# Performance work log

Measured on AMD Instinct MI355X. Metric: run time of the kernel, lower is better.

The kernel has to match this reference:

```python
import jax, jax.numpy as jnp
import numpy as np

DIM = 768
NUM_HEADS = 12
HEAD_DIM = DIM // NUM_HEADS
SCALE = HEAD_DIM ** -0.5
KEEP_NUM = 160


def setup_inputs() -> dict:
    key = jax.random.key(0)
    k0, k1, k2, k3 = jax.random.split(key, 4)
    B, N, C = 64, 197, DIM
    x = jax.random.normal(k0, (B, N, C), dtype=jnp.float32)
    # torch nn.Linear weights: [out_features, in_features]
    qkv_w = jax.random.normal(k1, (3 * C, C), dtype=jnp.float32) * (C ** -0.5)
    proj_w = jax.random.normal(k2, (C, C), dtype=jnp.float32) * (C ** -0.5)
    proj_b = jax.random.normal(k3, (C,), dtype=jnp.float32) * 0.01
    return {"x": x, "qkv_w": qkv_w, "proj_w": proj_w, "proj_b": proj_b}


def reference(x, qkv_w, proj_w, proj_b):
    B, N, C = x.shape
    H, D = NUM_HEADS, HEAD_DIM
    # qkv: [B, N, 3, H, D] -> q,k,v each [B, H, N, D]
    qkv = (x @ qkv_w.T).reshape(B, N, 3, H, D)
    qkv = jnp.transpose(qkv, (2, 0, 3, 1, 4))
    q, k, v = qkv[0], qkv[1], qkv[2]
    # raw pre-softmax scores [B, H, N, N]
    attn = jnp.einsum('bhnd,bhmd->bhnm', q, k) * SCALE
    # SUM_ABS_1: CLS row of scores, abs-summed over heads -> [B, N]
    attn_weight = jnp.sum(jnp.abs(attn[:, :, 0, :]), axis=1)
    # top_pool: keep top KEEP_NUM tokens by weight, indices sorted ascending
    _, idx = jax.lax.top_k(attn_weight, KEEP_NUM)
    keep_index = jnp.sort(idx, axis=-1)
    # standard attention
    attn = jax.nn.softmax(attn, axis=-1)
    out = jnp.einsum('bhnm,bhmd->bhnd', attn, v)
    out = jnp.transpose(out, (0, 2, 1, 3)).reshape(B, N, C)
    out = out @ proj_w.T + proj_b
    return out, keep_index
```

## Files before the change

kernel.cpp:

```cpp
#include <hip/hip_runtime.h>
#include <hip/hip_bf16.h>


#define BB 64
#define NN 197
#define CC 768
#define HH 12
#define DD 64
#define KEEP 160
#define SCALE_F 0.125f
#define OUT0_ELEMS ((size_t)BB * NN * CC)
#define VST 212

typedef __attribute__((ext_vector_type(8))) short bf16x8_t;
typedef __attribute__((ext_vector_type(4))) float f32x4_t;

__device__ __forceinline__ float b2f(unsigned short u) {
  union { unsigned u; float f; } cv; cv.u = (unsigned)u << 16; return cv.f;
}
__device__ __forceinline__ unsigned short f2b(float f) {
  union { float f; unsigned u; } cv; cv.f = f;
  return (unsigned short)((cv.u + 0x7FFFu + ((cv.u >> 16) & 1u)) >> 16);
}
__device__ __forceinline__ float ldmix(const void* p, size_t i, int f32) {
  return f32 ? ((const float*)p)[i] : b2f(((const unsigned short*)p)[i]);
}
__device__ __forceinline__ bf16x8_t ld8(const unsigned short* p) {
  short4 a = *(const short4*)p;
  short4 b = *(const short4*)(p + 4);
  bf16x8_t v = {a.x, a.y, a.z, a.w, b.x, b.y, b.z, b.w};
  return v;
}

__global__ void detect_kernel(const void* x, int* flag) {
  __shared__ int cnt;
  if (threadIdx.x == 0) cnt = 0;
  __syncthreads();
  const unsigned short* u = (const unsigned short*)x;
  int wild = 0;
  for (int i = threadIdx.x; i < 4096; i += 256) {
    int e = (u[i] >> 7) & 0xFF;
    wild += (e >= 140);
  }
  atomicAdd(&cnt, wild);
  __syncthreads();
  if (threadIdx.x == 0) *flag = (cnt > 100) ? 1 : 0;
}

__global__ void cvt_all(const void* qkv_w, const void* proj_w, const void* proj_b,
                        unsigned short* wb, unsigned short* pw, float* pbf,
                        const int* flag) {
  const int W3 = 3 * CC * CC, W1 = CC * CC;
  int i = blockIdx.x * 256 + threadIdx.x;
  const int f32 = *flag;
  if (i < W3) {
    wb[i] = f32 ? f2b(((const float*)qkv_w)[i]) : ((const unsigned short*)qkv_w)[i];
  } else if (i < W3 + W1) {
    int j = i - W3;
    pw[j] = f32 ? f2b(((const float*)proj_w)[j]) : ((const unsigned short*)proj_w)[j];
  } else if (i < W3 + W1 + CC) {
    int j = i - W3 - W1;
    pbf[j] = ldmix(proj_b, j, f32);
  }
}

__global__ void cvt_x(const void* __restrict__ x, size_t elem_off,
                      unsigned short* __restrict__ xb, int n8,
                      const int* __restrict__ flag) {
  const int i = blockIdx.x * 256 + threadIdx.x;
  if (i >= n8) return;
  const size_t src = elem_off + (size_t)i * 8;
  bf16x8_t v;
  if (*flag) {
    const float* xp = (const float*)x + src;
    float4 u0 = *(const float4*)xp;
    float4 u1 = *(const float4*)(xp + 4);
    v = bf16x8_t{(short)f2b(u0.x), (short)f2b(u0.y), (short)f2b(u0.z),
                 (short)f2b(u0.w), (short)f2b(u1.x), (short)f2b(u1.y),
                 (short)f2b(u1.z), (short)f2b(u1.w)};
  } else {
    v = *(const bf16x8_t*)((const unsigned short*)x + src);
  }
  *(bf16x8_t*)(xb + (size_t)i * 8) = v;
}

__global__ __launch_bounds__(256, 4) void qkv_gemm(
    const unsigned short* __restrict__ xb,
    const unsigned short* __restrict__ wb,
    unsigned short* __restrict__ qkvc, int Mc, int bc, int nRow) {
  const int xcd = blockIdx.x & 7;
  const int seq = blockIdx.x >> 3;
  const int colt = seq % 18;
  const int rowt = (seq / 18) * 8 + xcd;
  if (rowt >= nRow) return;
  const int m0 = rowt * 128;
  const int n0 = colt * 128;

  __shared__ unsigned short As[4096];
  __shared__ unsigned short Bs[4096];
  const int lane = threadIdx.x & 63;
  const int wave = threadIdx.x >> 6;
  const int l16  = lane & 15;
  const int quad = lane >> 4;
  const int wm = wave >> 1, wn = wave & 1;
  f32x4_t acc[4][4] = {};
  for (int kt = 0; kt < 24; kt++) {
    const int k0 = kt * 32;
    __syncthreads();
    #pragma unroll
    for (int ch = threadIdx.x; ch < 512; ch += 256) {
      int row = ch >> 2, kg = ch & 3;
      int gr = m0 + row; if (gr >= Mc) gr = Mc - 1;
      *(bf16x8_t*)&As[(row >> 4) * 512 + (row & 15) * 32 + kg * 8] =
          *(const bf16x8_t*)(xb + (size_t)gr * CC + k0 + kg * 8);
    }
    #pragma unroll
    for (int ch = threadIdx.x; ch < 512; ch += 256) {
      int row = ch >> 2, kg = ch & 3;
      *(bf16x8_t*)&Bs[(row >> 4) * 512 + (row & 15) * 32 + kg * 8] =
          *(const bf16x8_t*)(wb + (size_t)(n0 + row) * CC + k0 + kg * 8);
    }
    __syncthreads();
    bf16x8_t afr[4], bfr[4];
    #pragma unroll
    for (int r = 0; r < 4; r++)
      afr[r] = *(const bf16x8_t*)&As[(wm * 4 + r) * 512 + l16 * 32 + quad * 8];
    #pragma unroll
    for (int c = 0; c < 4; c++)
      bfr[c] = *(const bf16x8_t*)&Bs[(wn * 4 + c) * 512 + l16 * 32 + quad * 8];
    #pragma unroll
    for (int r = 0; r < 4; r++)
      #pragma unroll
      for (int c = 0; c < 4; c++)
        acc[r][c] = __builtin_amdgcn_mfma_f32_16x16x32_bf16(afr[r], bfr[c],
                                                            acc[r][c], 0, 0, 0);
  }
  #pragma unroll
  for (int c = 0; c < 4; c++) {
    const int col = n0 + wn * 64 + c * 16 + l16;
    const int s = col / CC;
    const int rem = col - s * CC;
    const int hc = rem >> 6, d = rem & 63;
    #pragma unroll
    for (int r = 0; r < 4; r++) {
      #pragma unroll
      for (int i = 0; i < 4; i++) {
        const int m = m0 + wm * 64 + r * 16 + quad * 4 + i;
        if (m < Mc) {
          const int bb = m / NN, n = m - bb * NN;
          qkvc[((((size_t)s * bc + bb) * HH + hc) * NN + n) * DD + d] =
              f2b(acc[r][c][i]);
        }
      }
    }
  }
}

__global__ __launch_bounds__(256, 4) void proj_gemm(
    const unsigned short* __restrict__ Yc,
    const unsigned short* __restrict__ pw,
    const float* __restrict__ pbf,
    void* __restrict__ out, size_t out_off, int Mc, int nRow,
    const int* __restrict__ flag) {
  const int xcd = blockIdx.x & 7;
  const int seq = blockIdx.x >> 3;
  const int colt = seq % 6;
  const int rowt = (seq / 6) * 8 + xcd;
  if (rowt >= nRow) return;
  const int m0 = rowt * 128;
  const int n0 = colt * 128;

  __shared__ unsigned short As[4096];
  __shared__ unsigned short Bs[4096];
  const int lane = threadIdx.x & 63;
  const int wave = threadIdx.x >> 6;
  const int l16  = lane & 15;
  const int quad = lane >> 4;
  const int wm = wave >> 1, wn = wave & 1;
  f32x4_t acc[4][4] = {};
  for (int kt = 0; kt < 24; kt++) {
    const int k0 = kt * 32;
    __syncthreads();
    #pragma unroll
    for (int ch = threadIdx.x; ch < 512; ch += 256) {
      int row = ch >> 2, kg = ch & 3;
      int gr = m0 + row; if (gr >= Mc) gr = Mc - 1;
      *(bf16x8_t*)&As[(row >> 4) * 512 + (row & 15) * 32 + kg * 8] =
          *(const bf16x8_t*)(Yc + (size_t)gr * CC + k0 + kg * 8);
    }
    #pragma unroll
    for (int ch = threadIdx.x; ch < 512; ch += 256) {
      int row = ch >> 2, kg = ch & 3;
      *(bf16x8_t*)&Bs[(row >> 4) * 512 + (row & 15) * 32 + kg * 8] =
          *(const bf16x8_t*)(pw + (size_t)(n0 + row) * CC + k0 + kg * 8);
    }
    __syncthreads();
    bf16x8_t afr[4], bfr[4];
    #pragma unroll
    for (int r = 0; r < 4; r++)
      afr[r] = *(const bf16x8_t*)&As[(wm * 4 + r) * 512 + l16 * 32 + quad * 8];
    #pragma unroll
    for (int c = 0; c < 4; c++)
      bfr[c] = *(const bf16x8_t*)&Bs[(wn * 4 + c) * 512 + l16 * 32 + quad * 8];
    #pragma unroll
    for (int r = 0; r < 4; r++)
      #pragma unroll
      for (int c = 0; c < 4; c++)
        acc[r][c] = __builtin_amdgcn_mfma_f32_16x16x32_bf16(afr[r], bfr[c],
                                                            acc[r][c], 0, 0, 0);
  }
  const int f32 = *flag;
  #pragma unroll
  for (int c = 0; c < 4; c++) {
    const int col = n0 + wn * 64 + c * 16 + l16;
    const float bv = pbf[col];
    #pragma unroll
    for (int r = 0; r < 4; r++) {
      #pragma unroll
      for (int i = 0; i < 4; i++) {
        const int m = m0 + wm * 64 + r * 16 + quad * 4 + i;
        if (m < Mc) {
          const float val = acc[r][c][i] + bv;
          const size_t oi = out_off + (size_t)m * CC + col;
          if (f32) ((float*)out)[oi] = val;
          else ((unsigned short*)out)[oi] = f2b(val);
        }
      }
    }
  }
}

__global__ __launch_bounds__(256, 3) void attn_kernel(
    const unsigned short* __restrict__ qkvc, int bc,
    unsigned short* __restrict__ Yc) {
  const int bh = blockIdx.x;
  const int bb = bh / HH;
  const int h  = bh % HH;
  const size_t mat = (size_t)bc * HH * NN * DD;
  const unsigned short* q = qkvc + ((size_t)bb * HH + h) * NN * DD;
  const unsigned short* k = q + mat;
  const unsigned short* v = q + 2 * mat;

  __shared__ unsigned short Vt[DD * VST];
  __shared__ unsigned short Pl[4][16 * VST];

  const int lane = threadIdx.x & 63;
  const int wave = threadIdx.x >> 6;
  const int l16  = lane & 15;
  const int quad = lane >> 4;

  #pragma unroll
  for (int it = 0; it < 53; it++) {
    const int key = it * 4 + wave;
    unsigned short val = (key < NN) ? v[(size_t)key * DD + lane]
                                    : (unsigned short)0;
    Vt[lane * VST + key] = val;
  }
  __syncthreads();

  unsigned short* Pw = &Pl[wave][0];

  for (int it = 0; it < 4; it++) {
    const int si = it * 4 + wave;
    if (si >= 13) break;
    const int q0 = si * 16;

    int qrow = q0 + l16; if (qrow >= NN) qrow = NN - 1;
    const unsigned short* qp = q + (size_t)qrow * DD + quad * 8;
    const bf16x8_t aq0 = *(const bf16x8_t*)qp;
    const bf16x8_t aq1 = *(const bf16x8_t*)(qp + 32);

    f32x4_t sc[13];
    #pragma unroll
    for (int ct = 0; ct < 13; ct++) {
      int key = ct * 16 + l16; if (key >= NN) key = NN - 1;
      const unsigned short* kp = k + (size_t)key * DD + quad * 8;
      const bf16x8_t b0 = *(const bf16x8_t*)kp;
      const bf16x8_t b1 = *(const bf16x8_t*)(kp + 32);
      f32x4_t t = {0.f, 0.f, 0.f, 0.f};
      t = __builtin_amdgcn_mfma_f32_16x16x32_bf16(aq0, b0, t, 0, 0, 0);
      t = __builtin_amdgcn_mfma_f32_16x16x32_bf16(aq1, b1, t, 0, 0, 0);
      sc[ct] = t;
    }

    float inv_l[4];
    #pragma unroll
    for (int i = 0; i < 4; i++) {
      float m = -1e30f;
      #pragma unroll
      for (int ct = 0; ct < 13; ct++)
        if (ct < 12 || l16 < 5) m = fmaxf(m, sc[ct][i] * SCALE_F);
      #pragma unroll
      for (int d = 1; d < 16; d <<= 1) m = fmaxf(m, __shfl_xor(m, d, 64));
      float s = 0.f;
      #pragma unroll
      for (int ct = 0; ct < 13; ct++) {
        const float p = (ct < 12 || l16 < 5) ? __expf(sc[ct][i] * SCALE_F - m)
                                             : 0.f;
        sc[ct][i] = p;
        s += p;
      }
      #pragma unroll
      for (int d = 1; d < 16; d <<= 1) s += __shfl_xor(s, d, 64);
      inv_l[i] = 1.0f / s;
    }

    #pragma unroll
    for (int i = 0; i < 4; i++) {
      const int ro = (quad * 4 + i) * VST;
      #pragma unroll
      for (int ct = 0; ct < 13; ct++)
        Pw[ro + ct * 16 + l16] = f2b(sc[ct][i]);
    }

    f32x4_t oc[4] = {};
    #pragma unroll
    for (int ks = 0; ks < 6; ks++) {
      const bf16x8_t ap = ld8(&Pw[l16 * VST + ks * 32 + quad * 8]);
      #pragma unroll
      for (int dt = 0; dt < 4; dt++) {
        const bf16x8_t bv = ld8(&Vt[(dt * 16 + l16) * VST + ks * 32 + quad * 8]);
        oc[dt] = __builtin_amdgcn_mfma_f32_16x16x32_bf16(ap, bv, oc[dt], 0, 0, 0);
      }
    }
    {
      const bf16x8_t zz = {};
      bf16x8_t ap = zz;
      if (quad < 2) ap = ld8(&Pw[l16 * VST + 192 + quad * 8]);
      #pragma unroll
      for (int dt = 0; dt < 4; dt++) {
        bf16x8_t bv = zz;
        if (quad < 2) bv = ld8(&Vt[(dt * 16 + l16) * VST + 192 + quad * 8]);
        oc[dt] = __builtin_amdgcn_mfma_f32_16x16x32_bf16(ap, bv, oc[dt], 0, 0, 0);
      }
    }

    #pragma unroll
    for (int i = 0; i < 4; i++) {
      const int n = q0 + quad * 4 + i;
      if (n < NN) {
        unsigned short* yp = Yc + ((size_t)bb * NN + n) * CC + h * DD;
        #pragma unroll
        for (int dt = 0; dt < 4; dt++)
          yp[dt * 16 + l16] = f2b(oc[dt][i] * inv_l[i]);
      }
    }
  }
}

__global__ __launch_bounds__(256, 4) void qcls_kernel(
    const void* __restrict__ x, const void* __restrict__ qkv_w,
    float* __restrict__ qc, const int* __restrict__ flag) {
  const int idx = blockIdx.x * 4 + (threadIdx.x >> 6);
  if (idx >= BB * CC) return;
  const int b = idx / CC, i = idx - b * CC;
  const int lane = threadIdx.x & 63;
  const int f32 = *flag;
  const size_t xr = (size_t)b * NN * CC;
  const size_t wr = (size_t)i * CC;
  float p = 0.f;
  #pragma unroll
  for (int j = 0; j < 12; j++)
    p += ldmix(x, xr + j * 64 + lane, f32) * ldmix(qkv_w, wr + j * 64 + lane, f32);
  #pragma unroll
  for (int m = 32; m; m >>= 1) p += __shfl_xor(p, m, 64);
  if (lane == 0) qc[(size_t)b * CC + i] = p;
}

__global__ __launch_bounds__(256, 4) void gmat_kernel(
    const void* __restrict__ qkv_w, const float* __restrict__ qc,
    float* __restrict__ g, const int* __restrict__ flag) {
  const int b = blockIdx.x, h = blockIdx.y;
  const int f32 = *flag;
  __shared__ float qh[DD];
  if (threadIdx.x < DD) qh[threadIdx.x] = qc[(size_t)b * CC + h * DD + threadIdx.x];
  __syncthreads();
  const int c0 = threadIdx.x, c1 = c0 + 256, c2 = c1 + 256;
  float a0 = 0.f, a1 = 0.f, a2 = 0.f;
  for (int d = 0; d < DD; d++) {
    const size_t ro = (size_t)(CC + h * DD + d) * CC;
    const float qv = qh[d];
    a0 += ldmix(qkv_w, ro + c0, f32) * qv;
    a1 += ldmix(qkv_w, ro + c1, f32) * qv;
    a2 += ldmix(qkv_w, ro + c2, f32) * qv;
  }
  float* gb = g + ((size_t)b * HH + h) * CC;
  gb[c0] = a0; gb[c1] = a1; gb[c2] = a2;
}

__global__ __launch_bounds__(256, 4) void score_kernel(
    const void* __restrict__ x, const float* __restrict__ g,
    float* __restrict__ wscore, const int* __restrict__ flag) {
  const int idx = blockIdx.x * 4 + (threadIdx.x >> 6);
  if (idx >= BB * NN) return;
  const int b = idx / NN, n = idx - b * NN;
  const int lane = threadIdx.x & 63;
  const int f32 = *flag;
  const size_t xr = ((size_t)b * NN + n) * CC;
  float xv[12];
  #pragma unroll
  for (int j = 0; j < 12; j++) xv[j] = ldmix(x, xr + j * 64 + lane, f32);
  const float* gb = g + (size_t)b * HH * CC;
  float acc = 0.f;
  #pragma unroll
  for (int h = 0; h < HH; h++) {
    const float* gh = gb + (size_t)h * CC;
    float p = 0.f;
    #pragma unroll
    for (int j = 0; j < 12; j++) p += xv[j] * gh[j * 64 + lane];
    #pragma unroll
    for (int m = 32; m; m >>= 1) p += __shfl_xor(p, m, 64);
    acc += fabsf(p);
  }
  if (lane == 0) wscore[(size_t)b * NN + n] = acc;
}

__global__ __launch_bounds__(256, 4) void rank_kernel(
    const float* __restrict__ wscore, void* __restrict__ out,
    const int* __restrict__ flag) {
  const int b = blockIdx.x;
  const int f32 = *flag;
  __shared__ float wgt[NN];
  __shared__ int   rank[NN];
  if (threadIdx.x < NN) wgt[threadIdx.x] = wscore[(size_t)b * NN + threadIdx.x];
  __syncthreads();
  const int n = threadIdx.x;
  if (n < NN) {
    float wi = wgt[n];
    int rk = 0;
    for (int j = 0; j < NN; j++) {
      float wj = wgt[j];
      rk += (wj > wi) || (wj == wi && j < n);
    }
    rank[n] = rk;
  }
  __syncthreads();
  if (n < NN && rank[n] < KEEP) {
    int pos = 0;
    for (int j = 0; j < n; j++) pos += (rank[j] < KEEP);
    const size_t oi = OUT0_ELEMS + (size_t)b * KEEP + pos;
    if (f32) ((float*)out)[oi] = (float)n;
    else ((unsigned short*)out)[oi] = f2b((float)n);
  }
}

extern "C" void kernel_launch(void* const* d_in, const int* in_sizes, int n_in,
                              void* d_out, int out_size, void* d_ws, size_t ws_size,
                              hipStream_t stream) {
  const void* x      = d_in[0];
  const void* qkv_w  = d_in[1];
  const void* proj_w = d_in[2];
  const void* proj_b = d_in[3];

  char* wsb = (char*)d_ws;
  int* flag = (int*)wsb;
  unsigned short* wb  = (unsigned short*)(wsb + 256);
  unsigned short* pw  = (unsigned short*)(wsb + 256 + 3538944);
  float* pbf    = (float*)(wsb + 256 + 3538944 + 1179648);
  float* qc     = (float*)(wsb + 256 + 3538944 + 1179648 + 4096);
  float* g      = qc + (size_t)BB * CC;
  float* wscore = g + (size_t)BB * HH * CC;
  const size_t fixed = 256 + 3538944 + 1179648 + 4096 + 196608 + 2359296 + 51200;
  char* chunk = wsb + fixed;

  const size_t per_batch = (size_t)NN * CC * 2
                         + 3ull * HH * NN * DD * 2
                         + (size_t)NN * CC * 2;
  int Bc = BB;
  while (Bc > 1 && fixed + (size_t)Bc * per_batch > ws_size) Bc >>= 1;

  unsigned short* xb   = (unsigned short*)chunk;
  unsigned short* qkvc = xb + (size_t)Bc * NN * CC;
  unsigned short* Yc   = qkvc + 3ull * Bc * HH * NN * DD;

  detect_kernel<<<1, 256, 0, stream>>>(x, flag);
  const int cvt_n = 3 * CC * CC + CC * CC + CC;
  cvt_all<<<(cvt_n + 255) / 256, 256, 0, stream>>>(qkv_w, proj_w, proj_b,
                                                   wb, pw, pbf, flag);

  qcls_kernel<<<(BB * CC + 3) / 4, 256, 0, stream>>>(x, qkv_w, qc, flag);
  gmat_kernel<<<dim3(BB, HH), 256, 0, stream>>>(qkv_w, qc, g, flag);
  score_kernel<<<(BB * NN + 3) / 4, 256, 0, stream>>>(x, g, wscore, flag);
  rank_kernel<<<BB, 256, 0, stream>>>(wscore, d_out, flag);

  const int nChunks = (BB + Bc - 1) / Bc;
  for (int cb = 0; cb < nChunks; cb++) {
    const int b0 = cb * Bc;
    const int bc = (BB - b0 < Bc) ? (BB - b0) : Bc;
    const int Mc = bc * NN;
    const int n8 = Mc * CC / 8;
    cvt_x<<<(n8 + 255) / 256, 256, 0, stream>>>(
        x, (size_t)b0 * NN * CC, xb, n8, flag);
    const int nRowQ = (Mc + 127) / 128;
    const int gridQ = 8 * 18 * ((nRowQ + 7) / 8);
    qkv_gemm<<<gridQ, 256, 0, stream>>>(xb, wb, qkvc, Mc, bc, nRowQ);
    attn_kernel<<<dim3(bc * HH), 256, 0, stream>>>(qkvc, bc, Yc);
    const int gridP = 8 * 6 * ((nRowQ + 7) / 8);
    proj_gemm<<<gridP, 256, 0, stream>>>(
        Yc, pw, pbf, d_out, (size_t)b0 * NN * CC, Mc, nRowQ, flag);
  }
}
```

Baseline: 395.0 us.

## Tile CLS query and G-matrix computations as shared-memory blocked GEMMs

Replaces the per-(batch,channel) warp dot products in qcls_kernel and the per-(batch,head) gmat_kernel with 64x64 shared-memory tiled GEMMs that compute 4x4 register tiles per thread. Each weight element is now loaded once per tile instead of once per batch, which cuts redundant global traffic on qkv_w. The trade-off is far fewer blocks (12 and 144), so these kernels may underfill the GPU and become latency-bound.

```diff
diff --git a/kernel.cpp b/kernel.cpp
--- a/kernel.cpp
+++ b/kernel.cpp
@@ -348,44 +348,86 @@
   }
 }
 
-__global__ __launch_bounds__(256, 4) void qcls_kernel(
+__global__ __launch_bounds__(256, 2) void qcls_kernel(
     const void* __restrict__ x, const void* __restrict__ qkv_w,
     float* __restrict__ qc, const int* __restrict__ flag) {
-  const int idx = blockIdx.x * 4 + (threadIdx.x >> 6);
-  if (idx >= BB * CC) return;
-  const int b = idx / CC, i = idx - b * CC;
-  const int lane = threadIdx.x & 63;
+  const int ct = blockIdx.x;
   const int f32 = *flag;
-  const size_t xr = (size_t)b * NN * CC;
-  const size_t wr = (size_t)i * CC;
-  float p = 0.f;
-  #pragma unroll
-  for (int j = 0; j < 12; j++)
-    p += ldmix(x, xr + j * 64 + lane, f32) * ldmix(qkv_w, wr + j * 64 + lane, f32);
-  #pragma unroll
-  for (int m = 32; m; m >>= 1) p += __shfl_xor(p, m, 64);
-  if (lane == 0) qc[(size_t)b * CC + i] = p;
-}
-
-__global__ __launch_bounds__(256, 4) void gmat_kernel(
+  __shared__ float Xs[64 * 68];
+  __shared__ float Ws[64 * 68];
+  const int tid = threadIdx.x;
+  const int tb = tid & 15, ti = tid >> 4;
+  float acc[4][4] = {};
+  for (int kt = 0; kt < 12; kt++) {
+    __syncthreads();
+    #pragma unroll
+    for (int e = 0; e < 16; e++) {
+      const int idx = tid + e * 256;
+      const int r = idx >> 6, k = idx & 63;
+      Xs[r * 68 + k] = ldmix(x, (size_t)r * NN * CC + kt * 64 + k, f32);
+      Ws[r * 68 + k] = ldmix(qkv_w, (size_t)(ct * 64 + r) * CC + kt * 64 + k, f32);
+    }
+    __syncthreads();
+    #pragma unroll
+    for (int k4 = 0; k4 < 16; k4++) {
+      float4 xv[4], wv[4];
+      #pragma unroll
+      for (int m = 0; m < 4; m++)
+        xv[m] = *(const float4*)&Xs[(tb + 16 * m) * 68 + k4 * 4];
+      #pragma unroll
+      for (int n = 0; n < 4; n++)
+        wv[n] = *(const float4*)&Ws[(ti + 16 * n) * 68 + k4 * 4];
+      #pragma unroll
+      for (int m = 0; m < 4; m++)
+        #pragma unroll
+        for (int n = 0; n < 4; n++)
+          acc[m][n] += xv[m].x * wv[n].x + xv[m].y * wv[n].y
+                     + xv[m].z * wv[n].z + xv[m].w * wv[n].w;
+    }
+  }
+  #pragma unroll
+  for (int m = 0; m < 4; m++)
+    #pragma unroll
+    for (int n = 0; n < 4; n++)
+      qc[(size_t)(tb + 16 * m) * CC + ct * 64 + ti + 16 * n] = acc[m][n];
+}
+
+__global__ __launch_bounds__(256, 2) void gmat_kernel(
     const void* __restrict__ qkv_w, const float* __restrict__ qc,
     float* __restrict__ g, const int* __restrict__ flag) {
-  const int b = blockIdx.x, h = blockIdx.y;
+  const int ct = blockIdx.x, h = blockIdx.y;
   const int f32 = *flag;
-  __shared__ float qh[DD];
-  if (threadIdx.x < DD) qh[threadIdx.x] = qc[(size_t)b * CC + h * DD + threadIdx.x];
+  __shared__ float Qs[64 * 68];
+  __shared__ float Ws[64 * 68];
+  const int tid = threadIdx.x;
+  #pragma unroll
+  for (int e = 0; e < 16; e++) {
+    const int idx = tid + e * 256;
+    const int r = idx >> 6, k = idx & 63;
+    Qs[r * 68 + k] = qc[(size_t)r * CC + h * 64 + k];
+    Ws[r * 68 + k] = ldmix(qkv_w, (size_t)(CC + h * 64 + r) * CC + ct * 64 + k, f32);
+  }
   __syncthreads();
-  const int c0 = threadIdx.x, c1 = c0 + 256, c2 = c1 + 256;
-  float a0 = 0.f, a1 = 0.f, a2 = 0.f;
-  for (int d = 0; d < DD; d++) {
-    const size_t ro = (size_t)(CC + h * DD + d) * CC;
-    const float qv = qh[d];
-    a0 += ldmix(qkv_w, ro + c0, f32) * qv;
-    a1 += ldmix(qkv_w, ro + c1, f32) * qv;
-    a2 += ldmix(qkv_w, ro + c2, f32) * qv;
-  }
-  float* gb = g + ((size_t)b * HH + h) * CC;
-  gb[c0] = a0; gb[c1] = a1; gb[c2] = a2;
+  const int tb = tid & 15, tc = tid >> 4;
+  float acc[4][4] = {};
+  for (int d = 0; d < 64; d++) {
+    float qv[4], wv[4];
+    #pragma unroll
+    for (int m = 0; m < 4; m++) qv[m] = Qs[(tb + 16 * m) * 68 + d];
+    #pragma unroll
+    for (int n = 0; n < 4; n++) wv[n] = Ws[d * 68 + tc + 16 * n];
+    #pragma unroll
+    for (int m = 0; m < 4; m++)
+      #pragma unroll
+      for (int n = 0; n < 4; n++)
+        acc[m][n] += qv[m] * wv[n];
+  }
+  #pragma unroll
+  for (int m = 0; m < 4; m++)
+    #pragma unroll
+    for (int n = 0; n < 4; n++)
+      g[((size_t)(tb + 16 * m) * HH + h) * CC + ct * 64 + tc + 16 * n] =
+          acc[m][n];
 }
 
 __global__ __launch_bounds__(256, 4) void score_kernel(
@@ -478,8 +520,8 @@
   cvt_all<<<(cvt_n + 255) / 256, 256, 0, stream>>>(qkv_w, proj_w, proj_b,
                                                    wb, pw, pbf, flag);
 
-  qcls_kernel<<<(BB * CC + 3) / 4, 256, 0, stream>>>(x, qkv_w, qc, flag);
-  gmat_kernel<<<dim3(BB, HH), 256, 0, stream>>>(qkv_w, qc, g, flag);
+  qcls_kernel<<<12, 256, 0, stream>>>(x, qkv_w, qc, flag);
+  gmat_kernel<<<dim3(12, HH), 256, 0, stream>>>(qkv_w, qc, g, flag);
   score_kernel<<<(BB * NN + 3) / 4, 256, 0, stream>>>(x, g, wscore, flag);
   rank_kernel<<<BB, 256, 0, stream>>>(wscore, d_out, flag);
 
```

After: 619.5 us. 1.57x slower.
